# Kernel tuning notes

Measured on AMD Instinct MI355X. Metric: run time of the kernel, lower is better.

## Reference

```python
import jax, jax.numpy as jnp
import numpy as np

B, S, H, NH = 1, 4096, 1024, 16
HD = H // NH  # head_dim = 64
ROPE_BASE = 10000.0


def setup_inputs() -> dict:
    key = jax.random.key(0)
    ks = jax.random.split(key, 8)
    sc = 0.02
    return {
        "hidden_states": jax.random.normal(ks[0], (B, S, H), jnp.float32),
        "attention_mask": jnp.zeros((B, 1, 1, S), jnp.float32),
        "Wq": jax.random.normal(ks[1], (H, H), jnp.float32) * sc,
        "bq": jnp.zeros((H,), jnp.float32),
        "Wk": jax.random.normal(ks[2], (H, H), jnp.float32) * sc,
        "bk": jnp.zeros((H,), jnp.float32),
        "Wv": jax.random.normal(ks[3], (H, H), jnp.float32) * sc,
        "bv": jnp.zeros((H,), jnp.float32),
    }


def _rope_tables(seq_len, head_dim, dtype):
    inv_freq = 1.0 / (ROPE_BASE ** (jnp.arange(0, head_dim, 2, dtype=jnp.float32) / head_dim))
    t = jnp.arange(seq_len, dtype=jnp.float32)
    freqs = jnp.einsum("s,d->sd", t, inv_freq)          # [S, HD/2]
    emb = jnp.concatenate([freqs, freqs], axis=-1)       # [S, HD]
    return jnp.cos(emb).astype(dtype), jnp.sin(emb).astype(dtype)


def _rotate_half(x):
    x1, x2 = jnp.split(x, 2, axis=-1)
    return jnp.concatenate([-x2, x1], axis=-1)


def reference(hidden_states, attention_mask, Wq, bq, Wk, bk, Wv, bv):
    bsz, q_len, _ = hidden_states.shape
    # QKV projections (torch Linear: x @ W.T + b), split into heads -> [B, NH, S, HD]
    def heads(x):
        return x.reshape(bsz, q_len, NH, HD).transpose(0, 2, 1, 3)
    q = heads(hidden_states @ Wq.T + bq)
    k = heads(hidden_states @ Wk.T + bk)
    v = heads(hidden_states @ Wv.T + bv)

    # RoPE with position_ids = arange(kv_seq_len)
    cos, sin = _rope_tables(q_len, HD, q.dtype)          # [S, HD]
    cos = cos[None, None]                                 # [1,1,S,HD]
    sin = sin[None, None]
    q = q * cos + _rotate_half(q) * sin
    k = k * cos + _rotate_half(k) * sin

    # Manual scaled-dot-product attention (baddbmm + softmax + matmul)
    scale = HD ** (-0.5)
    scores = jnp.einsum("bhqd,bhkd->bhqk", q, k) * scale  # [B,NH,S,S]
    scores = scores + attention_mask                      # broadcast additive mask
    weights = jax.nn.softmax(scores, axis=-1)
    attn = jnp.einsum("bhqk,bhkd->bhqd", weights, v)      # [B,NH,S,HD]

    # [B,S,NH,HD] -> [B,S,H]
    return attn.transpose(0, 2, 1, 3).reshape(bsz, q_len, NH * HD)
```

## Files before the change

### kernel.cpp

```cpp
#include <hip/hip_runtime.h>
#include <hip/hip_bf16.h>
#include <math.h>
#include <stdint.h>

#define S_ 4096
#define H_ 1024
#define NH_ 16
#define HD_ 64
#define LOG2E 1.4426950408889634f
#define QSCALE (0.125f * LOG2E)

typedef __bf16 bf16;
typedef __attribute__((ext_vector_type(8))) __bf16 bf16x8;
typedef __attribute__((ext_vector_type(4))) __bf16 bf16x4;
typedef __attribute__((ext_vector_type(4))) float f32x4;
typedef __attribute__((ext_vector_type(16))) float f32x16;
typedef __attribute__((ext_vector_type(2))) float f32x2;
typedef __attribute__((ext_vector_type(2))) int int2v;

__device__ __forceinline__ f32x4 mfma16(bf16x8 a, bf16x8 b, f32x4 c) {
    return __builtin_amdgcn_mfma_f32_16x16x32_bf16(a, b, c, 0, 0, 0);
}
__device__ __forceinline__ f32x16 mfma32(bf16x8 a, bf16x8 b, f32x16 c) {
    return __builtin_amdgcn_mfma_f32_32x32x16_bf16(a, b, c, 0, 0, 0);
}

__device__ __forceinline__ void gload16(const void* g, void* l) {
    __builtin_amdgcn_global_load_lds(
        (__attribute__((address_space(1))) void*)(uintptr_t)g,
        (__attribute__((address_space(3))) void*)(uintptr_t)l,
        16, 0, 0);
}

__device__ __forceinline__ unsigned cvtpk(float a, float b) {
    unsigned r;
    asm("v_cvt_pk_bf16_f32 %0, %1, %2" : "=v"(r) : "v"(a), "v"(b));
    return r;
}

__device__ __forceinline__ void swap32(unsigned a, unsigned b, unsigned& r0, unsigned& r1) {
#if __has_builtin(__builtin_amdgcn_permlane32_swap)
    int2v rr = __builtin_amdgcn_permlane32_swap((int)a, (int)b, false, false);
    r0 = (unsigned)rr[0];
    r1 = (unsigned)rr[1];
#else
    unsigned sa = (unsigned)__shfl_xor((int)a, 32, 64);
    unsigned sb = (unsigned)__shfl_xor((int)b, 32, 64);
    bool hi = (threadIdx.x & 32) != 0;
    r0 = hi ? sb : a;
    r1 = hi ? b : sa;
#endif
}

__device__ __forceinline__ float fexp2(float x) {
#if __has_builtin(__builtin_amdgcn_exp2f)
    return __builtin_amdgcn_exp2f(x);
#else
    return exp2f(x);
#endif
}

__global__ __launch_bounds__(256) void cvt_all_kernel(
    const float* __restrict__ hs, const float* __restrict__ Wq,
    const float* __restrict__ Wk, const float* __restrict__ Wv,
    const float* __restrict__ mask,
    bf16* __restrict__ Xb, bf16* __restrict__ Wqb,
    bf16* __restrict__ Wkb, bf16* __restrict__ Wvb,
    float2* __restrict__ tab, bf16* __restrict__ wM, float* __restrict__ wV) {
    int b = blockIdx.x;
    const float* src; bf16* dst; size_t base;
    if (b < 2048)      { src = hs; dst = Xb;  base = (size_t)b * 2048; }
    else if (b < 2560) { src = Wq; dst = Wqb; base = (size_t)(b - 2048) * 2048; }
    else if (b < 3072) { src = Wk; dst = Wkb; base = (size_t)(b - 2560) * 2048; }
    else               { src = Wv; dst = Wvb; base = (size_t)(b - 3072) * 2048; }
    size_t i = base + threadIdx.x * 8;
    float4 v0 = *reinterpret_cast<const float4*>(src + i);
    float4 v1 = *reinterpret_cast<const float4*>(src + i + 4);
    bf16x8 o;
    o[0] = (bf16)v0.x; o[1] = (bf16)v0.y; o[2] = (bf16)v0.z; o[3] = (bf16)v0.w;
    o[4] = (bf16)v1.x; o[5] = (bf16)v1.y; o[6] = (bf16)v1.z; o[7] = (bf16)v1.w;
    *reinterpret_cast<bf16x8*>(dst + i) = o;

    int idx = b * 256 + threadIdx.x;
    if (idx < S_ * 32) {
        int ii = idx & 31, s = idx >> 5;
        double ang = (double)s * exp(-(double)(2 * ii) / 64.0 * log(10000.0));
        tab[idx] = make_float2((float)cos(ang), (float)sin(ang));
    }
    if (idx < S_) {
        float e = exp2f(mask[idx] * LOG2E);
        bf16 eb = (bf16)e;
        wM[idx] = eb;
        wV[idx] = (float)eb;
    }
}

__global__ __launch_bounds__(256) void qkv_gemm_kernel(
    const bf16* __restrict__ Xb,
    const bf16* __restrict__ Wqb, const bf16* __restrict__ Wkb, const bf16* __restrict__ Wvb,
    const float* __restrict__ bqp, const float* __restrict__ bkp, const float* __restrict__ bvp,
    const float2* __restrict__ tab, const float* __restrict__ wV,
    bf16* __restrict__ Qo, bf16* __restrict__ Ko, bf16* __restrict__ Vto)
{
    __shared__ bf16 Alds[128 * 64];
    __shared__ bf16 Blds[128 * 64];
    const int z = blockIdx.z;
    const bf16* W = z == 0 ? Wqb : z == 1 ? Wkb : Wvb;
    const float* bias = z == 0 ? bqp : z == 1 ? bkp : bvp;
    const int tm = blockIdx.y * 128, tn = blockIdx.x * 128;
    const int tid = threadIdx.x, lane = tid & 63, wid = tid >> 6;
    const int wm = (wid >> 1) * 64, wn = (wid & 1) * 64;
    const int lr = lane & 15, lg = lane >> 4;
    const int c_row = tid >> 3, c_sub = tid & 7;

    f32x4 acc[4][4] = {};

    for (int kt = 0; kt < H_; kt += 64) {
        #pragma unroll
        for (int is = 0; is < 4; ++is) {
            int row = is * 32 + c_row;
            int sub = c_sub ^ (row & 7);
            gload16(&Xb[(size_t)(tm + row) * H_ + kt + sub * 8],
                    &Alds[(is * 256 + wid * 64) * 8]);
            gload16(&W[(size_t)(tn + row) * H_ + kt + sub * 8],
                    &Blds[(is * 256 + wid * 64) * 8]);
        }
        __syncthreads();

        #pragma unroll
        for (int kc = 0; kc < 2; ++kc) {
            bf16x8 af[4], bfr[4];
            #pragma unroll
            for (int mb = 0; mb < 4; ++mb) {
                int row = wm + mb * 16 + lr;
                int ch = (kc * 4 + lg) ^ (row & 7);
                af[mb] = *reinterpret_cast<const bf16x8*>(&Alds[row * 64 + ch * 8]);
            }
            #pragma unroll
            for (int nb = 0; nb < 4; ++nb) {
                int row = wn + nb * 16 + lr;
                int ch = (kc * 4 + lg) ^ (row & 7);
                bfr[nb] = *reinterpret_cast<const bf16x8*>(&Blds[row * 64 + ch * 8]);
            }
            #pragma unroll
            for (int mb = 0; mb < 4; ++mb)
                #pragma unroll
                for (int nb = 0; nb < 4; ++nb)
                    acc[mb][nb] = mfma16(af[mb], bfr[nb], acc[mb][nb]);
        }
        __syncthreads();
    }

    float bv4[4];
    #pragma unroll
    for (int nb = 0; nb < 4; ++nb) bv4[nb] = bias[tn + wn + nb * 16 + lr];

    if (z < 2) {
        bf16* Y = z == 0 ? Qo : Ko;
        const float fs = z == 0 ? QSCALE : 1.0f;
        #pragma unroll
        for (int mb = 0; mb < 4; ++mb) {
            #pragma unroll
            for (int r = 0; r < 4; ++r) {
                int row = tm + wm + mb * 16 + lg * 4 + r;
                #pragma unroll
                for (int nb = 0; nb < 2; ++nb) {
                    float2 cs = tab[row * 32 + nb * 16 + lr];
                    float x1 = acc[mb][nb][r] + bv4[nb];
                    float x2 = acc[mb][nb + 2][r] + bv4[nb + 2];
                    int col = tn + wn + nb * 16 + lr;
                    Y[(size_t)row * H_ + col]      = (bf16)((x1 * cs.x - x2 * cs.y) * fs);
                    Y[(size_t)row * H_ + col + 32] = (bf16)((x2 * cs.x + x1 * cs.y) * fs);
                }
            }
        }
    } else {
        #pragma unroll
        for (int mb = 0; mb < 4; ++mb) {
            int rowb = tm + wm + mb * 16 + lg * 4;
            float4 wv = *reinterpret_cast<const float4*>(&wV[rowb]);
            float wvr[4] = {wv.x, wv.y, wv.z, wv.w};
            #pragma unroll
            for (int nb = 0; nb < 4; ++nb) {
                int col = tn + wn + nb * 16 + lr;
                bf16x4 pk;
                #pragma unroll
                for (int r = 0; r < 4; ++r)
                    pk[r] = (bf16)((acc[mb][nb][r] + bv4[nb]) * wvr[r]);
                *reinterpret_cast<bf16x4*>(&Vto[(size_t)col * S_ + rowb]) = pk;
            }
        }
    }
}

__global__ __launch_bounds__(256) void attn_kernel(
    const bf16* __restrict__ Q, const bf16* __restrict__ K, const bf16* __restrict__ Vt,
    const bf16* __restrict__ wM, float* __restrict__ out)
{
    __shared__ bf16 Kl[2][64 * 64];
    __shared__ bf16 Vl[3][64 * 64];
    const int h = blockIdx.y;
    const int qb = blockIdx.x * 128;
    const int tid = threadIdx.x, lane = tid & 63, wid = tid >> 6;
    const int l31 = lane & 31, hi = lane >> 5;
    const int srow = wid * 8 + (lane >> 3);
    const int ssub = (lane & 7) ^ (srow & 7);

    if (blockIdx.x & 1) asm volatile("s_sleep 30");

    bf16x8 qf[4];
    {
        const bf16* qp = &Q[(size_t)(qb + wid * 32 + l31) * H_ + h * 64 + hi * 8];
        #pragma unroll
        for (int ks = 0; ks < 4; ++ks)
            qf[ks] = *reinterpret_cast<const bf16x8*>(qp + ks * 16);
    }

    f32x16 o0 = {}, o1 = {}, lacc = {};

    const bf16* kg = &K[(size_t)srow * H_ + h * 64 + ssub * 8];
    const bf16* vg = &Vt[(size_t)(h * 64 + srow) * S_ + ssub * 8];

    auto STAGE_K = [&](int buf) {
        gload16(kg,           &Kl[buf][(wid * 8) * 64]);
        gload16(kg + 32 * H_, &Kl[buf][(32 + wid * 8) * 64]);
        kg += 64 * H_;
    };
    auto STAGE_V = [&](int buf) {
        gload16(vg,           &Vl[buf][(wid * 8) * 64]);
        gload16(vg + 32 * S_, &Vl[buf][(32 + wid * 8) * 64]);
        vg += 64;
    };

    auto QK = [&](const bf16* Kb_, f32x16& q0, f32x16& q1) {
        f32x16 a = {}, b = {};
        __builtin_amdgcn_s_setprio(1);
        #pragma unroll
        for (int ks = 0; ks < 4; ++ks) {
            int ch = (2 * ks + hi) ^ (l31 & 7);
            bf16x8 kf0 = *reinterpret_cast<const bf16x8*>(&Kb_[l31 * 64 + ch * 8]);
            a = mfma32(kf0, qf[ks], a);
            bf16x8 kf1 = *reinterpret_cast<const bf16x8*>(&Kb_[(32 + l31) * 64 + ch * 8]);
            b = mfma32(kf1, qf[ks], b);
        }
        __builtin_amdgcn_s_setprio(0);
        q0 = a; q1 = b;
    };

    STAGE_K(0); STAGE_V(0);
    STAGE_K(1); STAGE_V(1);
    __syncthreads();

    f32x16 scA0, scA1, scB0, scB1;
    QK(Kl[0], scA0, scA1);

    int vstage = 2;
    int vread = 0;
    const bf16* wmt = wM + hi * 8;
    const int NT = S_ / 64;

    auto BODY = [&](int t, f32x16& sm0, f32x16& sm1, f32x16& qk0, f32x16& qk1) {
        __syncthreads();
        if (t + 1 < NT) QK(Kl[(t + 1) & 1], qk0, qk1);
        if (t + 2 < NT) {
            STAGE_K(t & 1);
            STAGE_V(vstage);
            vstage = vstage == 2 ? 0 : vstage + 1;
        }

        #pragma unroll
        for (int r = 0; r < 16; ++r) sm0[r] = fexp2(sm0[r]);
        #pragma unroll
        for (int r = 0; r < 16; ++r) sm1[r] = fexp2(sm1[r]);

        bf16x8 pf[4];
        #pragma unroll
        for (int ks = 0; ks < 2; ++ks) {
            unsigned w[4];
            #pragma unroll
            for (int wi = 0; wi < 2; ++wi) {
                unsigned u = cvtpk(sm0[8 * ks + 2 * wi],     sm0[8 * ks + 2 * wi + 1]);
                unsigned v = cvtpk(sm0[8 * ks + 4 + 2 * wi], sm0[8 * ks + 4 + 2 * wi + 1]);
                swap32(u, v, w[wi], w[wi + 2]);
            }
            union { unsigned u[4]; bf16x8 v; } cv;
            cv.u[0] = w[0]; cv.u[1] = w[1]; cv.u[2] = w[2]; cv.u[3] = w[3];
            pf[ks] = cv.v;
        }
        #pragma unroll
        for (int ks = 0; ks < 2; ++ks) {
            unsigned w[4];
            #pragma unroll
            for (int wi = 0; wi < 2; ++wi) {
                unsigned u = cvtpk(sm1[8 * ks + 2 * wi],     sm1[8 * ks + 2 * wi + 1]);
                unsigned v = cvtpk(sm1[8 * ks + 4 + 2 * wi], sm1[8 * ks + 4 + 2 * wi + 1]);
                swap32(u, v, w[wi], w[wi + 2]);
            }
            union { unsigned u[4]; bf16x8 v; } cv;
            cv.u[0] = w[0]; cv.u[1] = w[1]; cv.u[2] = w[2]; cv.u[3] = w[3];
            pf[2 + ks] = cv.v;
        }

        const bf16* Vb_ = Vl[vread];
        __builtin_amdgcn_s_setprio(1);
        #pragma unroll
        for (int ks = 0; ks < 4; ++ks) {
            int ch = (2 * ks + hi) ^ (l31 & 7);
            bf16x8 vf0 = *reinterpret_cast<const bf16x8*>(&Vb_[l31 * 64 + ch * 8]);
            o0 = mfma32(vf0, pf[ks], o0);
            bf16x8 vf1 = *reinterpret_cast<const bf16x8*>(&Vb_[(32 + l31) * 64 + ch * 8]);
            o1 = mfma32(vf1, pf[ks], o1);
            bf16x8 wf = *reinterpret_cast<const bf16x8*>(wmt + ks * 16);
            lacc = mfma32(wf, pf[ks], lacc);
        }
        __builtin_amdgcn_s_setprio(0);
        wmt += 64;
        vread = vread == 2 ? 0 : vread + 1;
    };

    for (int t = 0; t < NT; t += 2) {
        BODY(t,     scA0, scA1, scB0, scB1);
        BODY(t + 1, scB0, scB1, scA0, scA1);
    }

    float inv = 1.f / lacc[0];
    float* orow = &out[(size_t)(qb + wid * 32 + l31) * H_ + h * 64];
    #pragma unroll
    for (int g2 = 0; g2 < 4; ++g2) {
        float4 a, b;
        a.x = o0[g2 * 4 + 0] * inv; a.y = o0[g2 * 4 + 1] * inv;
        a.z = o0[g2 * 4 + 2] * inv; a.w = o0[g2 * 4 + 3] * inv;
        b.x = o1[g2 * 4 + 0] * inv; b.y = o1[g2 * 4 + 1] * inv;
        b.z = o1[g2 * 4 + 2] * inv; b.w = o1[g2 * 4 + 3] * inv;
        *reinterpret_cast<float4*>(orow + 8 * g2 + 4 * hi) = a;
        *reinterpret_cast<float4*>(orow + 32 + 8 * g2 + 4 * hi) = b;
    }
}

extern "C" void kernel_launch(void* const* d_in, const int* in_sizes, int n_in,
                              void* d_out, int out_size, void* d_ws, size_t ws_size,
                              hipStream_t stream) {
    const float* hs   = (const float*)d_in[0];
    const float* mask = (const float*)d_in[1];
    const float* Wq   = (const float*)d_in[2];
    const float* bq   = (const float*)d_in[3];
    const float* Wk   = (const float*)d_in[4];
    const float* bk   = (const float*)d_in[5];
    const float* Wv   = (const float*)d_in[6];
    const float* bv   = (const float*)d_in[7];
    float* out = (float*)d_out;

    char* ws = (char*)d_ws;
    bf16* Xb    = (bf16*)(ws);
    bf16* Wqb   = (bf16*)(ws + (8u  << 20));
    bf16* Wkb   = (bf16*)(ws + (10u << 20));
    bf16* Wvb   = (bf16*)(ws + (12u << 20));
    bf16* Qb    = (bf16*)(ws + (14u << 20));
    bf16* Kb    = (bf16*)(ws + (22u << 20));
    bf16* Vt    = (bf16*)(ws + (30u << 20));
    float2* tab = (float2*)(ws + (38u << 20));
    bf16* wM    = (bf16*)(ws + (39u << 20));
    float* wV   = (float*)(ws + (39u << 20) + 65536);

    cvt_all_kernel<<<3584, 256, 0, stream>>>(hs, Wq, Wk, Wv, mask,
                                             Xb, Wqb, Wkb, Wvb, tab, wM, wV);
    qkv_gemm_kernel<<<dim3(H_ / 128, S_ / 128, 3), 256, 0, stream>>>(
        Xb, Wqb, Wkb, Wvb, bq, bk, bv, tab, wV, Qb, Kb, Vt);
    attn_kernel<<<dim3(S_ / 128, NH_), 256, 0, stream>>>(Qb, Kb, Vt, wM, out);
}
```

Baseline: 152.8 us.

## Split attention KV range across two blocks and add a combine kernel

Adds a split-KV mode: each (query-block, head) pair is processed by two blocks, each covering half the key/value tiles and writing unnormalized partial outputs and row sums to workspace. A new combine kernel adds the two partials and normalizes. The attention loop is also simplified from a software-pipelined QK-ahead scheme with triple-buffered V to a plain double-buffered loop, with launch bounds raised to 4 waves and the s_sleep stagger removed. The split doubles the grid from 512 blocks to 1024 to improve CU occupancy, at the cost of extra global traffic for partials, an extra launch, and less intra-block overlap.

```diff
diff --git a/kernel.cpp b/kernel.cpp
--- a/kernel.cpp
+++ b/kernel.cpp
@@ -193,20 +193,24 @@
     }
 }
 
-__global__ __launch_bounds__(256) void attn_kernel(
+template<int NSPLIT>
+__global__ __launch_bounds__(256, 4) void attn_kernel(
     const bf16* __restrict__ Q, const bf16* __restrict__ K, const bf16* __restrict__ Vt,
-    const bf16* __restrict__ wM, float* __restrict__ out)
+    const bf16* __restrict__ wM, float* __restrict__ out,
+    float* __restrict__ opart, float* __restrict__ lpart)
 {
     __shared__ bf16 Kl[2][64 * 64];
-    __shared__ bf16 Vl[3][64 * 64];
+    __shared__ bf16 Vl[2][64 * 64];
     const int h = blockIdx.y;
     const int qb = blockIdx.x * 128;
+    const int z = blockIdx.z;
     const int tid = threadIdx.x, lane = tid & 63, wid = tid >> 6;
     const int l31 = lane & 31, hi = lane >> 5;
     const int srow = wid * 8 + (lane >> 3);
     const int ssub = (lane & 7) ^ (srow & 7);
 
-    if (blockIdx.x & 1) asm volatile("s_sleep 30");
+    const int NT = S_ / 64;
+    const int t0 = z * (NT / NSPLIT), t1 = t0 + NT / NSPLIT;
 
     bf16x8 qf[4];
     {
@@ -218,60 +222,43 @@
 
     f32x16 o0 = {}, o1 = {}, lacc = {};
 
-    const bf16* kg = &K[(size_t)srow * H_ + h * 64 + ssub * 8];
-    const bf16* vg = &Vt[(size_t)(h * 64 + srow) * S_ + ssub * 8];
-
-    auto STAGE_K = [&](int buf) {
+    const bf16* kg = &K[(size_t)(t0 * 64 + srow) * H_ + h * 64 + ssub * 8];
+    const bf16* vg = &Vt[(size_t)(h * 64 + srow) * S_ + t0 * 64 + ssub * 8];
+
+    auto STAGE = [&](int buf) {
         gload16(kg,           &Kl[buf][(wid * 8) * 64]);
         gload16(kg + 32 * H_, &Kl[buf][(32 + wid * 8) * 64]);
-        kg += 64 * H_;
-    };
-    auto STAGE_V = [&](int buf) {
         gload16(vg,           &Vl[buf][(wid * 8) * 64]);
         gload16(vg + 32 * S_, &Vl[buf][(32 + wid * 8) * 64]);
+        kg += 64 * H_;
         vg += 64;
     };
 
-    auto QK = [&](const bf16* Kb_, f32x16& q0, f32x16& q1) {
-        f32x16 a = {}, b = {};
+    STAGE(0);
+    __syncthreads();
+    int cur = 0;
+    const bf16* wmt = wM + t0 * 64 + hi * 8;
+
+    for (int t = t0; t < t1; ++t) {
+        if (t + 1 < t1) STAGE(cur ^ 1);
+
+        f32x16 sc0 = {}, sc1 = {};
+        const bf16* Kb_ = Kl[cur];
         __builtin_amdgcn_s_setprio(1);
         #pragma unroll
         for (int ks = 0; ks < 4; ++ks) {
             int ch = (2 * ks + hi) ^ (l31 & 7);
             bf16x8 kf0 = *reinterpret_cast<const bf16x8*>(&Kb_[l31 * 64 + ch * 8]);
-            a = mfma32(kf0, qf[ks], a);
+            sc0 = mfma32(kf0, qf[ks], sc0);
             bf16x8 kf1 = *reinterpret_cast<const bf16x8*>(&Kb_[(32 + l31) * 64 + ch * 8]);
-            b = mfma32(kf1, qf[ks], b);
+            sc1 = mfma32(kf1, qf[ks], sc1);
         }
         __builtin_amdgcn_s_setprio(0);
-        q0 = a; q1 = b;
-    };
-
-    STAGE_K(0); STAGE_V(0);
-    STAGE_K(1); STAGE_V(1);
-    __syncthreads();
-
-    f32x16 scA0, scA1, scB0, scB1;
-    QK(Kl[0], scA0, scA1);
-
-    int vstage = 2;
-    int vread = 0;
-    const bf16* wmt = wM + hi * 8;
-    const int NT = S_ / 64;
-
-    auto BODY = [&](int t, f32x16& sm0, f32x16& sm1, f32x16& qk0, f32x16& qk1) {
-        __syncthreads();
-        if (t + 1 < NT) QK(Kl[(t + 1) & 1], qk0, qk1);
-        if (t + 2 < NT) {
-            STAGE_K(t & 1);
-            STAGE_V(vstage);
-            vstage = vstage == 2 ? 0 : vstage + 1;
-        }
-
-        #pragma unroll
-        for (int r = 0; r < 16; ++r) sm0[r] = fexp2(sm0[r]);
-        #pragma unroll
-        for (int r = 0; r < 16; ++r) sm1[r] = fexp2(sm1[r]);
+
+        #pragma unroll
+        for (int r = 0; r < 16; ++r) sc0[r] = fexp2(sc0[r]);
+        #pragma unroll
+        for (int r = 0; r < 16; ++r) sc1[r] = fexp2(sc1[r]);
 
         bf16x8 pf[4];
         #pragma unroll
@@ -279,8 +266,8 @@
             unsigned w[4];
             #pragma unroll
             for (int wi = 0; wi < 2; ++wi) {
-                unsigned u = cvtpk(sm0[8 * ks + 2 * wi],     sm0[8 * ks + 2 * wi + 1]);
-                unsigned v = cvtpk(sm0[8 * ks + 4 + 2 * wi], sm0[8 * ks + 4 + 2 * wi + 1]);
+                unsigned u = cvtpk(sc0[8 * ks + 2 * wi],     sc0[8 * ks + 2 * wi + 1]);
+                unsigned v = cvtpk(sc0[8 * ks + 4 + 2 * wi], sc0[8 * ks + 4 + 2 * wi + 1]);
                 swap32(u, v, w[wi], w[wi + 2]);
             }
             union { unsigned u[4]; bf16x8 v; } cv;
@@ -292,8 +279,8 @@
             unsigned w[4];
             #pragma unroll
             for (int wi = 0; wi < 2; ++wi) {
-                unsigned u = cvtpk(sm1[8 * ks + 2 * wi],     sm1[8 * ks + 2 * wi + 1]);
-                unsigned v = cvtpk(sm1[8 * ks + 4 + 2 * wi], sm1[8 * ks + 4 + 2 * wi + 1]);
+                unsigned u = cvtpk(sc1[8 * ks + 2 * wi],     sc1[8 * ks + 2 * wi + 1]);
+                unsigned v = cvtpk(sc1[8 * ks + 4 + 2 * wi], sc1[8 * ks + 4 + 2 * wi + 1]);
                 swap32(u, v, w[wi], w[wi + 2]);
             }
             union { unsigned u[4]; bf16x8 v; } cv;
@@ -301,7 +288,7 @@
             pf[2 + ks] = cv.v;
         }
 
-        const bf16* Vb_ = Vl[vread];
+        const bf16* Vb_ = Vl[cur];
         __builtin_amdgcn_s_setprio(1);
         #pragma unroll
         for (int ks = 0; ks < 4; ++ks) {
@@ -315,26 +302,60 @@
         }
         __builtin_amdgcn_s_setprio(0);
         wmt += 64;
-        vread = vread == 2 ? 0 : vread + 1;
-    };
-
-    for (int t = 0; t < NT; t += 2) {
-        BODY(t,     scA0, scA1, scB0, scB1);
-        BODY(t + 1, scB0, scB1, scA0, scA1);
-    }
-
-    float inv = 1.f / lacc[0];
-    float* orow = &out[(size_t)(qb + wid * 32 + l31) * H_ + h * 64];
-    #pragma unroll
-    for (int g2 = 0; g2 < 4; ++g2) {
-        float4 a, b;
-        a.x = o0[g2 * 4 + 0] * inv; a.y = o0[g2 * 4 + 1] * inv;
-        a.z = o0[g2 * 4 + 2] * inv; a.w = o0[g2 * 4 + 3] * inv;
-        b.x = o1[g2 * 4 + 0] * inv; b.y = o1[g2 * 4 + 1] * inv;
-        b.z = o1[g2 * 4 + 2] * inv; b.w = o1[g2 * 4 + 3] * inv;
-        *reinterpret_cast<float4*>(orow + 8 * g2 + 4 * hi) = a;
-        *reinterpret_cast<float4*>(orow + 32 + 8 * g2 + 4 * hi) = b;
-    }
+
+        __syncthreads();
+        cur ^= 1;
+    }
+
+    const int q = qb + wid * 32 + l31;
+    if (NSPLIT == 1) {
+        float inv = 1.f / lacc[0];
+        float* orow = &out[(size_t)q * H_ + h * 64];
+        #pragma unroll
+        for (int g2 = 0; g2 < 4; ++g2) {
+            float4 a, b;
+            a.x = o0[g2 * 4 + 0] * inv; a.y = o0[g2 * 4 + 1] * inv;
+            a.z = o0[g2 * 4 + 2] * inv; a.w = o0[g2 * 4 + 3] * inv;
+            b.x = o1[g2 * 4 + 0] * inv; b.y = o1[g2 * 4 + 1] * inv;
+            b.z = o1[g2 * 4 + 2] * inv; b.w = o1[g2 * 4 + 3] * inv;
+            *reinterpret_cast<float4*>(orow + 8 * g2 + 4 * hi) = a;
+            *reinterpret_cast<float4*>(orow + 32 + 8 * g2 + 4 * hi) = b;
+        }
+    } else {
+        float* op = &opart[(((size_t)z * NH_ + h) * S_ + q) * 64];
+        #pragma unroll
+        for (int g2 = 0; g2 < 4; ++g2) {
+            float4 a, b;
+            a.x = o0[g2 * 4 + 0]; a.y = o0[g2 * 4 + 1];
+            a.z = o0[g2 * 4 + 2]; a.w = o0[g2 * 4 + 3];
+            b.x = o1[g2 * 4 + 0]; b.y = o1[g2 * 4 + 1];
+            b.z = o1[g2 * 4 + 2]; b.w = o1[g2 * 4 + 3];
+            *reinterpret_cast<float4*>(op + 8 * g2 + 4 * hi) = a;
+            *reinterpret_cast<float4*>(op + 32 + 8 * g2 + 4 * hi) = b;
+        }
+        if (hi == 0)
+            lpart[((size_t)z * NH_ + h) * S_ + q] = lacc[0];
+    }
+}
+
+__global__ __launch_bounds__(256) void combine_kernel(const float* __restrict__ opart,
+                                                      const float* __restrict__ lpart,
+                                                      float* __restrict__ out) {
+    int idx = blockIdx.x * 256 + threadIdx.x;
+    int d4 = idx & 15;
+    int q = (idx >> 4) & 4095;
+    int h = idx >> 16;
+    float l0 = lpart[(size_t)h * S_ + q];
+    float l1 = lpart[((size_t)NH_ + h) * S_ + q];
+    float inv = 1.f / (l0 + l1);
+    float4 a = *reinterpret_cast<const float4*>(&opart[(((size_t)h) * S_ + q) * 64 + d4 * 4]);
+    float4 b = *reinterpret_cast<const float4*>(&opart[(((size_t)NH_ + h) * S_ + q) * 64 + d4 * 4]);
+    float4 r;
+    r.x = (a.x + b.x) * inv;
+    r.y = (a.y + b.y) * inv;
+    r.z = (a.z + b.z) * inv;
+    r.w = (a.w + b.w) * inv;
+    *reinterpret_cast<float4*>(&out[(size_t)q * H_ + h * 64 + d4 * 4]) = r;
 }
 
 extern "C" void kernel_launch(void* const* d_in, const int* in_sizes, int n_in,
@@ -361,10 +382,21 @@
     float2* tab = (float2*)(ws + (38u << 20));
     bf16* wM    = (bf16*)(ws + (39u << 20));
     float* wV   = (float*)(ws + (39u << 20) + 65536);
+    float* opart = (float*)(ws + (40u << 20));
+    float* lpart = (float*)(ws + (72u << 20));
+    const size_t NEED = (size_t)73u << 20;
 
     cvt_all_kernel<<<3584, 256, 0, stream>>>(hs, Wq, Wk, Wv, mask,
                                              Xb, Wqb, Wkb, Wvb, tab, wM, wV);
     qkv_gemm_kernel<<<dim3(H_ / 128, S_ / 128, 3), 256, 0, stream>>>(
         Xb, Wqb, Wkb, Wvb, bq, bk, bv, tab, wV, Qb, Kb, Vt);
-    attn_kernel<<<dim3(S_ / 128, NH_), 256, 0, stream>>>(Qb, Kb, Vt, wM, out);
-}
+
+    if (ws_size >= NEED) {
+        attn_kernel<2><<<dim3(S_ / 128, NH_, 2), 256, 0, stream>>>(
+            Qb, Kb, Vt, wM, out, opart, lpart);
+        combine_kernel<<<(S_ * NH_ * 16) / 256, 256, 0, stream>>>(opart, lpart, out);
+    } else {
+        attn_kernel<1><<<dim3(S_ / 128, NH_, 1), 256, 0, stream>>>(
+            Qb, Kb, Vt, wM, out, nullptr, nullptr);
+    }
+}
```

Measured after the change: 155.5 us. No clear change (+1.8%).
